# Optimization experiments

Measured on AMD Instinct MI355X. Metric: run time of the kernel, lower is better.

The kernel has to match this reference:

```python
import jax, jax.numpy as jnp
import numpy as np

D = 512; H = 8; NL = 8; V = 258; W = 8; DFF = 4 * D; DH = D // H


def setup_inputs() -> dict:
    key = jax.random.key(0)
    ks = jax.random.split(key, 20)
    B, L = 8, 1024
    s = 0.02
    n = lambda k, shp: (jax.random.normal(k, shp, jnp.float32) * s)
    x = jax.random.randint(ks[0], (B, L), 0, 256)
    return dict(
        x=x,
        embed=n(ks[1], (V, D)),
        ep_w=n(ks[2], (D, 1)), ep_b=jnp.zeros((D,), jnp.float32),
        in_w=n(ks[3], (NL, 3 * D, D)), in_b=jnp.zeros((NL, 3 * D), jnp.float32),
        op_w=n(ks[4], (NL, D, D)), op_b=jnp.zeros((NL, D), jnp.float32),
        ln1_w=jnp.ones((NL, D), jnp.float32), ln1_b=jnp.zeros((NL, D), jnp.float32),
        ln2_w=jnp.ones((NL, D), jnp.float32), ln2_b=jnp.zeros((NL, D), jnp.float32),
        f1_w=n(ks[5], (NL, DFF, D)), f1_b=jnp.zeros((NL, DFF), jnp.float32),
        f2_w=n(ks[6], (NL, D, DFF)), f2_b=jnp.zeros((NL, D), jnp.float32),
        out_w=n(ks[7], (V, D)),
    )


def _layer_norm(x, w, b, eps=1e-5):
    mu = jnp.mean(x, -1, keepdims=True)
    var = jnp.mean(jnp.square(x - mu), -1, keepdims=True)
    return (x - mu) * jax.lax.rsqrt(var + eps) * w + b


def _entropy_features(x):
    # Sliding-window byte histogram entropy (same math as one-hot.sum over window)
    B, L = x.shape
    oh = jax.nn.one_hot(x, V, dtype=jnp.float32)          # [B,L,V]
    oh = oh.at[..., 256:].set(0.0)                        # special tokens zeroed
    cs = jnp.cumsum(oh, axis=1)
    cs = jnp.concatenate([jnp.zeros_like(cs[:, :1]), cs], axis=1)
    counts = cs[:, W:] - cs[:, :-W]                       # [B, L-W+1, V]
    probs = jnp.clip(counts / W, 1e-10)
    ent = -jnp.sum(probs * (jnp.log(probs) / jnp.log(2.0)), -1, keepdims=True)
    return jnp.pad(ent, ((0, 0), (0, W - 1), (0, 0)))     # [B,L,1]


def _block(h, in_w, in_b, op_w, op_b, ln1_w, ln1_b, ln2_w, ln2_b, f1_w, f1_b, f2_w, f2_b):
    B, L, _ = h.shape
    g = _layer_norm(h, ln1_w, ln1_b)
    qkv = g @ in_w.T + in_b                               # [B,L,3D]
    q, k, v = jnp.split(qkv, 3, axis=-1)
    q = q.reshape(B, L, H, DH); k = k.reshape(B, L, H, DH); v = v.reshape(B, L, H, DH)
    scores = jnp.einsum('blhd,bmhd->bhlm', q, k) / np.sqrt(DH).astype(np.float32)
    attn = jax.nn.softmax(scores, axis=-1)
    o = jnp.einsum('bhlm,bmhd->blhd', attn, v).reshape(B, L, D)
    h = h + o @ op_w.T + op_b
    g = _layer_norm(h, ln2_w, ln2_b)
    h = h + jax.nn.gelu(g @ f1_w.T + f1_b, approximate=False) @ f2_w.T + f2_b
    return h


def reference(x, embed, ep_w, ep_b, in_w, in_b, op_w, op_b, ln1_w, ln1_b,
              ln2_w, ln2_b, f1_w, f1_b, f2_w, f2_b, out_w):
    ent = _entropy_features(x)                            # [B,L,1]
    h = embed[x] + ent @ ep_w.T + ep_b                    # [B,L,D]
    for i in range(NL // 2):                              # local encoder layers
        h = _block(h, in_w[i], in_b[i], op_w[i], op_b[i], ln1_w[i], ln1_b[i],
                   ln2_w[i], ln2_b[i], f1_w[i], f1_b[i], f2_w[i], f2_b[i])
    for i in range(NL // 2, NL):                          # global transformer layers
        h = _block(h, in_w[i], in_b[i], op_w[i], op_b[i], ln1_w[i], ln1_b[i],
                   ln2_w[i], ln2_b[i], f1_w[i], f1_b[i], f2_w[i], f2_b[i])
    return h @ out_w.T                                    # [B,L,V]
```

## Files before the change

### kernel.cpp

```cpp
#include <hip/hip_runtime.h>
#include <hip/hip_bf16.h>

#define D_MODEL 512
#define NHEAD   8
#define DHEAD   64
#define SEQ     1024
#define NBATCH  8
#define NTOK    8192
#define DFF_N   2048
#define NLAYER  8
#define VOCAB   258
#define VPAD    384

typedef float f32x4 __attribute__((ext_vector_type(4)));
typedef short s16x8 __attribute__((ext_vector_type(8)));

__device__ __forceinline__ ushort f2b(float f) {
    union { float f; unsigned u; } v; v.f = f;
    unsigned r = (v.u + 0x7fffu + ((v.u >> 16) & 1u)) >> 16;
    return (ushort)r;
}
__device__ __forceinline__ float gelu_f(float x) {
    return 0.5f * x * (1.0f + erff(x * 0.70710678118654752f));
}
__device__ __forceinline__ void gl_lds16(const void* g, void* l) {
    __builtin_amdgcn_global_load_lds(
        (const __attribute__((address_space(1))) void*)g,
        (__attribute__((address_space(3))) void*)l, 16, 0, 0);
}
__device__ __forceinline__ float exp2_fast(float x) {
    float r; asm("v_exp_f32 %0, %1" : "=v"(r) : "v"(x)); return r;
}
__device__ __forceinline__ unsigned cvtpk(float lo, float hi) {
    unsigned r; asm("v_cvt_pk_bf16_f32 %0, %1, %2" : "=v"(r) : "v"(lo), "v"(hi)); return r;
}

__global__ __launch_bounds__(256) void cvt_bf16(
    const float* __restrict__ in, ushort* __restrict__ out, int n)
{
    int i = (blockIdx.x * 256 + threadIdx.x) << 2;
    if (i >= n) return;
    float4 v = *(const float4*)(in + i);
    ushort4 o;
    o.x = f2b(v.x); o.y = f2b(v.y); o.z = f2b(v.z); o.w = f2b(v.w);
    *(ushort4*)(out + i) = o;
}

__global__ __launch_bounds__(256) void cvt_layer(
    const float* __restrict__ s0, const float* __restrict__ s1,
    const float* __restrict__ s2, const float* __restrict__ s3,
    ushort* __restrict__ d0, ushort* __restrict__ d1,
    ushort* __restrict__ d2, ushort* __restrict__ d3)
{
    int i = (blockIdx.x * 256 + threadIdx.x) << 2;
    const float* s; ushort* d; int off;
    if (i < 786432)        { s = s0; d = d0; off = i; }
    else if (i < 1048576)  { s = s1; d = d1; off = i - 786432; }
    else if (i < 2097152)  { s = s2; d = d2; off = i - 1048576; }
    else                   { s = s3; d = d3; off = i - 2097152; }
    float4 v = *(const float4*)(s + off);
    ushort4 o;
    o.x = f2b(v.x); o.y = f2b(v.y); o.z = f2b(v.z); o.w = f2b(v.w);
    *(ushort4*)(d + off) = o;
}

__global__ __launch_bounds__(128) void embed_kernel(
    const int* __restrict__ x, const float* __restrict__ embed,
    const float* __restrict__ ep_w, const float* __restrict__ ep_b,
    float* __restrict__ h)
{
    int t = blockIdx.x;
    int pos = t & (SEQ - 1);
    float ent = 0.0f;
    if (pos <= SEQ - 8) {
        int v[8];
        #pragma unroll
        for (int i = 0; i < 8; i++) v[i] = x[t + i];
        float s = 0.0f;
        #pragma unroll
        for (int i = 0; i < 8; i++) {
            int c = 0;
            #pragma unroll
            for (int j = 0; j < 8; j++) c += (v[j] == v[i]) ? 1 : 0;
            s += log2f((float)c);
        }
        ent = 3.0f - 0.125f * s;
    }
    int tok = x[t];
    int d = threadIdx.x << 2;
    float e[4], w[4], bb[4], r[4];
    *(float4*)e  = *(const float4*)(embed + (size_t)tok * D_MODEL + d);
    *(float4*)w  = *(const float4*)(ep_w + d);
    *(float4*)bb = *(const float4*)(ep_b + d);
    #pragma unroll
    for (int j = 0; j < 4; j++) r[j] = e[j] + ent * w[j] + bb[j];
    *(float4*)(h + (size_t)t * D_MODEL + d) = *(float4*)r;
}

__global__ __launch_bounds__(256) void ln_kernel(
    const float* __restrict__ in, const float* __restrict__ w,
    const float* __restrict__ b, ushort* __restrict__ out)
{
    int wid = threadIdx.x >> 6, lane = threadIdx.x & 63;
    int t = (blockIdx.x << 2) + wid;
    const float* row = in + (size_t)t * D_MODEL;
    float a[8];
    *(float4*)(a)     = *(const float4*)(row + (lane << 2));
    *(float4*)(a + 4) = *(const float4*)(row + 256 + (lane << 2));
    float s = 0.f;
    #pragma unroll
    for (int j = 0; j < 8; j++) s += a[j];
    #pragma unroll
    for (int o = 1; o < 64; o <<= 1) s += __shfl_xor(s, o);
    float mu = s * (1.0f / 512.0f);
    float vs = 0.f;
    #pragma unroll
    for (int j = 0; j < 8; j++) { float d0 = a[j] - mu; vs += d0 * d0; }
    #pragma unroll
    for (int o = 1; o < 64; o <<= 1) vs += __shfl_xor(vs, o);
    float inv = rsqrtf(vs * (1.0f / 512.0f) + 1e-5f);
    float ww[8], bbv[8];
    *(float4*)(ww)      = *(const float4*)(w + (lane << 2));
    *(float4*)(ww + 4)  = *(const float4*)(w + 256 + (lane << 2));
    *(float4*)(bbv)     = *(const float4*)(b + (lane << 2));
    *(float4*)(bbv + 4) = *(const float4*)(b + 256 + (lane << 2));
    ushort* orow = out + (size_t)t * D_MODEL;
    ushort4 o1, o2;
    o1.x = f2b((a[0] - mu) * inv * ww[0] + bbv[0]);
    o1.y = f2b((a[1] - mu) * inv * ww[1] + bbv[1]);
    o1.z = f2b((a[2] - mu) * inv * ww[2] + bbv[2]);
    o1.w = f2b((a[3] - mu) * inv * ww[3] + bbv[3]);
    o2.x = f2b((a[4] - mu) * inv * ww[4] + bbv[4]);
    o2.y = f2b((a[5] - mu) * inv * ww[5] + bbv[5]);
    o2.z = f2b((a[6] - mu) * inv * ww[6] + bbv[6]);
    o2.w = f2b((a[7] - mu) * inv * ww[7] + bbv[7]);
    *(ushort4*)(orow + (lane << 2))       = o1;
    *(ushort4*)(orow + 256 + (lane << 2)) = o2;
}

template<int BN>
__global__ __launch_bounds__(256) void gemm_t(
    const ushort* __restrict__ A, const ushort* __restrict__ Bw,
    const float* __restrict__ bias, const float* __restrict__ resid,
    float* __restrict__ Cf, ushort* __restrict__ Cb, ushort* __restrict__ Vtr,
    int M, int N, int K, int fuse)
{
    constexpr int NF = BN / 32;
    constexpr int EPW = BN + 4;
    __shared__ ushort SMEM[2 * 4096 + 2 * BN * 32];
    ushort* As0 = SMEM;
    ushort* Bs0 = SMEM + 8192;
    const int tid = threadIdx.x;
    const int l = tid & 63, w = tid >> 6;
    const int m0 = blockIdx.x << 7, n0 = blockIdx.y * BN;
    const int wrn = (w >> 1) << 6;
    const int wcn = (w & 1) * (BN / 2);
    const int fm = l & 15, fk8 = (l >> 4) << 3;
    f32x4 acc[4][NF] = {};

    const ushort* ga0 = A + (size_t)(m0 + (w << 5) + (l >> 2)) * K + ((l & 3) << 3);
    const ushort* ga1 = ga0 + (size_t)16 * K;
    const ushort* gb0;
    const ushort* gb1 = nullptr;
    if constexpr (BN == 128) {
        gb0 = Bw + (size_t)(n0 + (w << 5) + (l >> 2)) * K + ((l & 3) << 3);
        gb1 = gb0 + (size_t)16 * K;
    } else {
        gb0 = Bw + (size_t)(n0 + (w << 4) + (l >> 2)) * K + ((l & 3) << 3);
    }

    const int nk = K >> 5;
    auto stage = [&](int buf, int ko) {
        gl_lds16(ga0 + ko, As0 + buf * 4096 + (w << 10));
        gl_lds16(ga1 + ko, As0 + buf * 4096 + (w << 10) + 512);
        if constexpr (BN == 128) {
            gl_lds16(gb0 + ko, Bs0 + buf * (BN * 32) + (w << 10));
            gl_lds16(gb1 + ko, Bs0 + buf * (BN * 32) + (w << 10) + 512);
        } else {
            gl_lds16(gb0 + ko, Bs0 + buf * (BN * 32) + (w << 9));
        }
    };

    stage(0, 0);
    __syncthreads();
    int cur = 0;
    for (int kt = 0; kt < nk; ++kt) {
        if (kt + 1 < nk) stage(cur ^ 1, (kt + 1) << 5);
        s16x8 af[4], bf[NF];
        #pragma unroll
        for (int x = 0; x < 4; ++x)
            af[x] = *(const s16x8*)&As0[cur * 4096 + (wrn + (x << 4) + fm) * 32 + fk8];
        #pragma unroll
        for (int y = 0; y < NF; ++y)
            bf[y] = *(const s16x8*)&Bs0[cur * (BN * 32) + (wcn + (y << 4) + fm) * 32 + fk8];
        #pragma unroll
        for (int x = 0; x < 4; ++x)
            #pragma unroll
            for (int y = 0; y < NF; ++y)
                acc[x][y] = __builtin_amdgcn_mfma_f32_16x16x32_bf16(
                    af[x], bf[y], acc[x][y], 0, 0, 0);
        __syncthreads();
        cur ^= 1;
    }

    const float qs = (Vtr && n0 < 512) ? 0.18033688011112042f : 1.0f;
    const bool vblk = (Vtr != nullptr) && (n0 >= 1024);

    if (Cb != nullptr || vblk) {
        float* Ep = (float*)SMEM;
        const int lrw = ((w >> 1) << 4) + ((l >> 4) << 2);
        #pragma unroll
        for (int x = 0; x < 4; ++x) {
            __syncthreads();
            #pragma unroll
            for (int y = 0; y < NF; ++y) {
                const int c = wcn + (y << 4) + fm;
                const float bv = bias ? bias[n0 + c] : 0.f;
                #pragma unroll
                for (int i = 0; i < 4; ++i) {
                    float v = acc[x][y][i] + bv;
                    v *= qs;
                    if (fuse == 1) v = gelu_f(v);
                    Ep[(lrw + i) * EPW + c] = v;
                }
            }
            __syncthreads();
            if (vblk) {
                const int c = tid & 127;
                const int run = tid >> 7;
                const int colg = (n0 - 1024) + c;
                const int hh = colg >> 6, dd = colg & 63;
                float v16[16];
                #pragma unroll
                for (int j = 0; j < 16; ++j)
                    v16[j] = Ep[((run << 4) + j) * EPW + c];
                unsigned pk[8];
                #pragma unroll
                for (int j = 0; j < 8; ++j) pk[j] = cvtpk(v16[2 * j], v16[2 * j + 1]);
                ushort* dst = Vtr + ((size_t)(((m0 >> 10) << 3) + hh) * 64 + dd) * 1024
                              + (m0 & 1023) + (run << 6) + (x << 4);
                *(uint4*)dst       = *(uint4*)(pk);
                *(uint4*)(dst + 8) = *(uint4*)(pk + 4);
            } else {
                constexpr int TPR = BN / 8;
                constexpr int RPP = 256 / TPR;
                constexpr int NP = 32 / RPP;
                #pragma unroll
                for (int p = 0; p < NP; ++p) {
                    const int lr = p * RPP + (tid / TPR);
                    const int cg = (tid % TPR) << 3;
                    const int grow = m0 + ((lr >> 4) << 6) + (x << 4) + (lr & 15);
                    const int gcol = n0 + cg;
                    float v8[8];
                    *(float4*)(v8)     = *(float4*)&Ep[lr * EPW + cg];
                    *(float4*)(v8 + 4) = *(float4*)&Ep[lr * EPW + cg + 4];
                    if (fuse == 2) {
                        float4 r1 = *(const float4*)&resid[(size_t)grow * N + gcol];
                        float4 r2 = *(const float4*)&resid[(size_t)grow * N + gcol + 4];
                        v8[0] += r1.x; v8[1] += r1.y; v8[2] += r1.z; v8[3] += r1.w;
                        v8[4] += r2.x; v8[5] += r2.y; v8[6] += r2.z; v8[7] += r2.w;
                    }
                    if (Cf) {
                        *(float4*)&Cf[(size_t)grow * N + gcol]     = *(float4*)v8;
                        *(float4*)&Cf[(size_t)grow * N + gcol + 4] = *(float4*)(v8 + 4);
                    }
                    unsigned pk[4];
                    pk[0] = cvtpk(v8[0], v8[1]); pk[1] = cvtpk(v8[2], v8[3]);
                    pk[2] = cvtpk(v8[4], v8[5]); pk[3] = cvtpk(v8[6], v8[7]);
                    *(uint4*)&Cb[(size_t)grow * N + gcol] = *(uint4*)pk;
                }
            }
        }
        return;
    }

    const int col0 = n0 + wcn + fm;
    const int row0 = m0 + wrn + ((l >> 4) << 2);
    #pragma unroll
    for (int x = 0; x < 4; ++x) {
        #pragma unroll
        for (int y = 0; y < NF; ++y) {
            int col = col0 + (y << 4);
            if (col >= N) continue;
            float bv = bias ? bias[col] : 0.f;
            #pragma unroll
            for (int i = 0; i < 4; ++i) {
                int row = row0 + (x << 4) + i;
                float v = acc[x][y][i] + bv;
                if (fuse == 1) v = gelu_f(v);
                else if (fuse == 2) v += resid[(size_t)row * N + col];
                Cf[(size_t)row * N + col] = v;
            }
        }
    }
}

__global__ __launch_bounds__(256) void attn_mfma(
    const ushort* __restrict__ qkv, const ushort* __restrict__ vT,
    ushort* __restrict__ out)
{
    __shared__ ushort Ks[2][4096];
    __shared__ ushort Vs[2][4096];
    const int tid = threadIdx.x;
    const int l = tid & 63, w = tid >> 6;
    const int p = blockIdx.y * gridDim.x + blockIdx.x;
    const int bh = ((p & 7) << 3) + ((p >> 3) >> 4);
    const int q0 = ((p >> 3) & 15) << 6;
    const int b = bh >> 3, h = bh & 7;
    const ushort* base = qkv + (size_t)b * SEQ * 1536 + h * 64;
    const ushort* kg = base + 512;
    const ushort* vg = vT + ((size_t)bh << 16);
    const int fm = l & 15, fk = l >> 4;

    s16x8 qf[2];
    {
        const ushort* qrow = base + (size_t)(q0 + (w << 4) + fm) * 1536 + (fk << 3);
        qf[0] = *(const s16x8*)qrow;
        qf[1] = *(const s16x8*)(qrow + 32);
    }
    s16x8 ones_f;
    #pragma unroll
    for (int j = 0; j < 8; ++j) ones_f[j] = (short)0x3F80;

    f32x4 accO[4] = {};
    f32x4 accL = {};

    const int rr = l >> 3;
    const int cch = ((l & 7) ^ rr) << 3;
    const ushort* kga = kg + (size_t)((w << 4) + rr) * 1536 + cch;
    const ushort* kgb = kga + (size_t)8 * 1536;
    const ushort* vga = vg + (size_t)((w << 4) + rr) * 1024 + cch;
    const ushort* vgb = vga + (size_t)8 * 1024;

    int fidx[2][4];
    #pragma unroll
    for (int ks = 0; ks < 2; ++ks)
        #pragma unroll
        for (int n = 0; n < 4; ++n)
            fidx[ks][n] = (((n << 4) + fm) << 6) + ((((ks << 2) + fk) ^ (l & 7)) << 3);

    const int srcA = ((fk & 1) << 5) + fm;
    const int srcB = srcA + 16;
    const bool hiN = (fk >> 1) != 0;

    #define STAGE(buf, kt)                                                    \
        do {                                                                  \
            ushort* ka_ = &Ks[buf][w << 10];                                  \
            ushort* va_ = &Vs[buf][w << 10];                                  \
            gl_lds16(kga + (size_t)((kt) << 6) * 1536, ka_);                  \
            gl_lds16(kgb + (size_t)((kt) << 6) * 1536, ka_ + 512);            \
            gl_lds16(vga + ((kt) << 6), va_);                                 \
            gl_lds16(vgb + ((kt) << 6), va_ + 512);                           \
        } while (0)

    STAGE(0, 0);
    asm volatile("s_waitcnt vmcnt(0)" ::: "memory");
    __builtin_amdgcn_s_barrier();

    int cur = 0;
    for (int kt = 0; kt < SEQ / 64; ++kt) {
        if (kt + 1 < SEQ / 64) STAGE(cur ^ 1, kt + 1);
        __builtin_amdgcn_sched_barrier(0);

        f32x4 s[4] = {};
        __builtin_amdgcn_s_setprio(1);
        #pragma unroll
        for (int ks = 0; ks < 2; ++ks)
            #pragma unroll
            for (int n = 0; n < 4; ++n) {
                s16x8 kf = *(const s16x8*)&Ks[cur][fidx[ks][n]];
                s[n] = __builtin_amdgcn_mfma_f32_16x16x32_bf16(kf, qf[ks], s[n], 0, 0, 0);
            }
        __builtin_amdgcn_s_setprio(0);

        unsigned pk0[2], pk1[2], pk2[2], pk3[2];
        pk0[0] = cvtpk(exp2_fast(s[0][0]), exp2_fast(s[0][1]));
        pk0[1] = cvtpk(exp2_fast(s[0][2]), exp2_fast(s[0][3]));
        pk1[0] = cvtpk(exp2_fast(s[1][0]), exp2_fast(s[1][1]));
        pk1[1] = cvtpk(exp2_fast(s[1][2]), exp2_fast(s[1][3]));
        pk2[0] = cvtpk(exp2_fast(s[2][0]), exp2_fast(s[2][1]));
        pk2[1] = cvtpk(exp2_fast(s[2][2]), exp2_fast(s[2][3]));
        pk3[0] = cvtpk(exp2_fast(s[3][0]), exp2_fast(s[3][1]));
        pk3[1] = cvtpk(exp2_fast(s[3][2]), exp2_fast(s[3][3]));

        #pragma unroll
        for (int ks = 0; ks < 2; ++ks) {
            unsigned u0 = ks ? pk2[0] : pk0[0], u1 = ks ? pk2[1] : pk0[1];
            unsigned v0 = ks ? pk3[0] : pk1[0], v1 = ks ? pk3[1] : pk1[1];
            unsigned a0 = __shfl((int)u0, srcA), b0 = __shfl((int)v0, srcA);
            unsigned a1 = __shfl((int)u1, srcA), b1 = __shfl((int)v1, srcA);
            unsigned a2 = __shfl((int)u0, srcB), b2 = __shfl((int)v0, srcB);
            unsigned a3 = __shfl((int)u1, srcB), b3 = __shfl((int)v1, srcB);
            union { unsigned u[4]; s16x8 v; } pb;
            pb.u[0] = hiN ? b0 : a0;
            pb.u[1] = hiN ? b1 : a1;
            pb.u[2] = hiN ? b2 : a2;
            pb.u[3] = hiN ? b3 : a3;
            __builtin_amdgcn_s_setprio(1);
            #pragma unroll
            for (int n = 0; n < 4; ++n) {
                s16x8 vf = *(const s16x8*)&Vs[cur][fidx[ks][n]];
                accO[n] = __builtin_amdgcn_mfma_f32_16x16x32_bf16(vf, pb.v, accO[n], 0, 0, 0);
            }
            accL = __builtin_amdgcn_mfma_f32_16x16x32_bf16(ones_f, pb.v, accL, 0, 0, 0);
            __builtin_amdgcn_s_setprio(0);
        }

        asm volatile("s_waitcnt vmcnt(0)" ::: "memory");
        __builtin_amdgcn_s_barrier();
        __builtin_amdgcn_sched_barrier(0);
        cur ^= 1;
    }
    #undef STAGE

    const int q = q0 + (w << 4) + fm;
    float inv = 1.0f / accL[0];
    ushort* obase = out + ((size_t)(b * SEQ + q)) * 512 + h * 64 + (fk << 2);
    #pragma unroll
    for (int n = 0; n < 4; ++n) {
        ushort4 o;
        o.x = f2b(accO[n][0] * inv);
        o.y = f2b(accO[n][1] * inv);
        o.z = f2b(accO[n][2] * inv);
        o.w = f2b(accO[n][3] * inv);
        *(ushort4*)(obase + (n << 4)) = o;
    }
}

extern "C" void kernel_launch(void* const* d_in, const int* in_sizes, int n_in,
                              void* d_out, int out_size, void* d_ws, size_t ws_size,
                              hipStream_t stream) {
    const int*   x     = (const int*)  d_in[0];
    const float* embed = (const float*)d_in[1];
    const float* ep_w  = (const float*)d_in[2];
    const float* ep_b  = (const float*)d_in[3];
    const float* in_w  = (const float*)d_in[4];
    const float* in_b  = (const float*)d_in[5];
    const float* op_w  = (const float*)d_in[6];
    const float* op_b  = (const float*)d_in[7];
    const float* ln1_w = (const float*)d_in[8];
    const float* ln1_b = (const float*)d_in[9];
    const float* ln2_w = (const float*)d_in[10];
    const float* ln2_b = (const float*)d_in[11];
    const float* f1_w  = (const float*)d_in[12];
    const float* f1_b  = (const float*)d_in[13];
    const float* f2_w  = (const float*)d_in[14];
    const float* f2_b  = (const float*)d_in[15];
    const float* out_w = (const float*)d_in[16];
    float* out = (float*)d_out;

    char* ws = (char*)d_ws;
    float*  h    = (float*) (ws + 0);
    ushort* g    = (ushort*)(ws + 16777216);
    ushort* big  = (ushort*)(ws + 25165824);
    ushort* qkvb = big;
    ushort* hb   = (ushort*)(ws + 58720256);
    ushort* wq   = (ushort*)(ws + 67108864);
    ushort* wo   = (ushort*)(ws + 68681728);
    ushort* w1   = (ushort*)(ws + 69206016);
    ushort* w2   = (ushort*)(ws + 71303168);
    ushort* wv   = (ushort*)(ws + 73400320);
    ushort* vT   = (ushort*)(ws + 73793536);

    hipMemsetAsync(wv, 0, (size_t)VPAD * 512 * 2, stream);
    cvt_bf16<<<(VOCAB * 512 / 4 + 255) / 256, 256, 0, stream>>>(out_w, wv, VOCAB * 512);

    embed_kernel<<<NTOK, 128, 0, stream>>>(x, embed, ep_w, ep_b, h);

    for (int l = 0; l < NLAYER; ++l) {
        cvt_layer<<<3072, 256, 0, stream>>>(
            in_w + (size_t)l * 786432, op_w + (size_t)l * 262144,
            f1_w + (size_t)l * 1048576, f2_w + (size_t)l * 1048576,
            wq, wo, w1, w2);

        ln_kernel<<<NTOK / 4, 256, 0, stream>>>(h, ln1_w + l * 512, ln1_b + l * 512, g);
        gemm_t<128><<<dim3(64, 12), 256, 0, stream>>>(g, wq, in_b + l * 1536, nullptr,
                                                      nullptr, qkvb, vT, NTOK, 1536, 512, 0);
        attn_mfma<<<dim3(SEQ / 64, 64), 256, 0, stream>>>(qkvb, vT, g);
        gemm_t<64><<<dim3(64, 8), 256, 0, stream>>>(g, wo, op_b + l * 512, h,
                                                    h, nullptr, nullptr, NTOK, 512, 512, 2);
        ln_kernel<<<NTOK / 4, 256, 0, stream>>>(h, ln2_w + l * 512, ln2_b + l * 512, g);
        gemm_t<128><<<dim3(64, 16), 256, 0, stream>>>(g, w1, f1_b + l * 2048, nullptr,
                                                      nullptr, big, nullptr, NTOK, 2048, 512, 1);
        gemm_t<64><<<dim3(64, 8), 256, 0, stream>>>(big, w2, f2_b + l * 512, h,
                                                    h, (l == NLAYER - 1) ? hb : nullptr, nullptr,
                                                    NTOK, 512, 2048, 2);
    }

    gemm_t<64><<<dim3(64, 5), 256, 0, stream>>>(hb, wv, nullptr, nullptr,
                                                out, nullptr, nullptr, NTOK, VOCAB, 512, 0);
}
```

Before: 1.402 ms.

## Load GEMM B fragments directly from global into registers, skip LDS staging

The GEMM no longer stages the weight (B) tile through shared memory. Each wave loads its B fragments straight from global memory into registers, double-buffered in two register sets, while A is still staged through LDS with the main loop unrolled by two. This shrinks LDS use, which may allow higher occupancy, and removes the LDS write/read round trip for B. In exchange, B reads are no longer shared between waves, so global and L2 traffic rises and register pressure grows.

Result: slower. 1.875 ms (+33.8%).

```diff
diff --git a/kernel.cpp b/kernel.cpp
--- a/kernel.cpp
+++ b/kernel.cpp
@@ -147,9 +147,9 @@
 {
     constexpr int NF = BN / 32;
     constexpr int EPW = BN + 4;
-    __shared__ ushort SMEM[2 * 4096 + 2 * BN * 32];
-    ushort* As0 = SMEM;
-    ushort* Bs0 = SMEM + 8192;
+    constexpr int SMEMF = (32 * EPW > 4096) ? 32 * EPW : 4096;
+    __shared__ float SMEMf[SMEMF];
+    ushort* As0 = (ushort*)SMEMf;
     const int tid = threadIdx.x;
     const int l = tid & 63, w = tid >> 6;
     const int m0 = blockIdx.x << 7, n0 = blockIdx.y * BN;
@@ -160,54 +160,49 @@
 
     const ushort* ga0 = A + (size_t)(m0 + (w << 5) + (l >> 2)) * K + ((l & 3) << 3);
     const ushort* ga1 = ga0 + (size_t)16 * K;
-    const ushort* gb0;
-    const ushort* gb1 = nullptr;
-    if constexpr (BN == 128) {
-        gb0 = Bw + (size_t)(n0 + (w << 5) + (l >> 2)) * K + ((l & 3) << 3);
-        gb1 = gb0 + (size_t)16 * K;
-    } else {
-        gb0 = Bw + (size_t)(n0 + (w << 4) + (l >> 2)) * K + ((l & 3) << 3);
-    }
+    const ushort* gB  = Bw + (size_t)(n0 + wcn + fm) * K + fk8;
 
     const int nk = K >> 5;
-    auto stage = [&](int buf, int ko) {
-        gl_lds16(ga0 + ko, As0 + buf * 4096 + (w << 10));
-        gl_lds16(ga1 + ko, As0 + buf * 4096 + (w << 10) + 512);
-        if constexpr (BN == 128) {
-            gl_lds16(gb0 + ko, Bs0 + buf * (BN * 32) + (w << 10));
-            gl_lds16(gb1 + ko, Bs0 + buf * (BN * 32) + (w << 10) + 512);
-        } else {
-            gl_lds16(gb0 + ko, Bs0 + buf * (BN * 32) + (w << 9));
-        }
+    auto stageA = [&](int buf, int ko) {
+        gl_lds16(ga0 + ko, As0 + (buf << 12) + (w << 10));
+        gl_lds16(ga1 + ko, As0 + (buf << 12) + (w << 10) + 512);
     };
-
-    stage(0, 0);
-    __syncthreads();
-    int cur = 0;
-    for (int kt = 0; kt < nk; ++kt) {
-        if (kt + 1 < nk) stage(cur ^ 1, (kt + 1) << 5);
-        s16x8 af[4], bf[NF];
+    auto loadB = [&](s16x8* d, int ko) {
+        #pragma unroll
+        for (int y = 0; y < NF; ++y)
+            d[y] = *(const s16x8*)(gB + (size_t)(y << 4) * K + ko);
+    };
+    auto mfmaStep = [&](int buf, const s16x8* bf) {
+        s16x8 af[4];
         #pragma unroll
         for (int x = 0; x < 4; ++x)
-            af[x] = *(const s16x8*)&As0[cur * 4096 + (wrn + (x << 4) + fm) * 32 + fk8];
-        #pragma unroll
-        for (int y = 0; y < NF; ++y)
-            bf[y] = *(const s16x8*)&Bs0[cur * (BN * 32) + (wcn + (y << 4) + fm) * 32 + fk8];
+            af[x] = *(const s16x8*)&As0[(buf << 12) + (wrn + (x << 4) + fm) * 32 + fk8];
         #pragma unroll
         for (int x = 0; x < 4; ++x)
             #pragma unroll
             for (int y = 0; y < NF; ++y)
                 acc[x][y] = __builtin_amdgcn_mfma_f32_16x16x32_bf16(
                     af[x], bf[y], acc[x][y], 0, 0, 0);
+    };
+
+    s16x8 bfA[NF], bfB[NF];
+    stageA(0, 0);
+    loadB(bfA, 0);
+    __syncthreads();
+    for (int kt = 0; kt < nk; kt += 2) {
+        if (kt + 1 < nk) { stageA(1, (kt + 1) << 5); loadB(bfB, (kt + 1) << 5); }
+        mfmaStep(0, bfA);
         __syncthreads();
-        cur ^= 1;
+        if (kt + 2 < nk) { stageA(0, (kt + 2) << 5); loadB(bfA, (kt + 2) << 5); }
+        if (kt + 1 < nk) mfmaStep(1, bfB);
+        __syncthreads();
     }
 
     const float qs = (Vtr && n0 < 512) ? 0.18033688011112042f : 1.0f;
     const bool vblk = (Vtr != nullptr) && (n0 >= 1024);
 
     if (Cb != nullptr || vblk) {
-        float* Ep = (float*)SMEM;
+        float* Ep = SMEMf;
         const int lrw = ((w >> 1) << 4) + ((l >> 4) << 2);
         #pragma unroll
         for (int x = 0; x < 4; ++x) {
```
